# Optimization experiments

Hardware: AMD Instinct MI355X
Metric: run time of the kernel (lower is better)

## Reference

```python
import jax, jax.numpy as jnp
import numpy as np

B, T, H = 32, 512, 1024   # batch, seq, hidden
L = 512                   # max_seq_length (must be <= 512 for rel_pos_bias)
E = 2048                  # hidden * expansion_factor
S = 128                   # shared qk dim
SQRT_S = float(np.sqrt(S))
EPS = 1e-5


def setup_inputs() -> dict:
    key = jax.random.key(0)
    ks = jax.random.split(key, 9)
    return {
        "x": jax.random.normal(ks[0], (B, T, H), jnp.float32),
        "ln_w": jnp.ones((H,), jnp.float32),
        "ln_b": jnp.zeros((H,), jnp.float32),
        "uv_w": jax.random.normal(ks[1], (2 * E + S, H), jnp.float32) * 0.02,  # torch Linear [out,in]
        "uv_b": jnp.zeros((2 * E + S,), jnp.float32),
        "gamma": jax.random.uniform(ks[2], (2, S), jnp.float32),
        "beta": jax.random.uniform(ks[3], (2, S), jnp.float32),
        "w": jax.random.uniform(ks[4], (2 * L - 1,), jnp.float32),  # Toeplitz rel-pos table
        "o_w": jax.random.normal(ks[5], (H, E), jnp.float32) * 0.02,
        "o_b": jnp.zeros((H,), jnp.float32),
    }


def _rope(x):
    # x: [B, T, 2, S]; positions run along the seq dim (dim=1), faithful to GAU.rope
    half = x.shape[-1] // 2
    pos = jnp.arange(x.shape[1], dtype=x.dtype)
    # note: original uses 10000**(+i/half) (increasing freq) — keep it faithful
    inv_freq = 10000.0 ** (jnp.arange(half, dtype=x.dtype) / half)
    sinusoid = pos[:, None] * inv_freq[None, :]          # [T, half]
    sin = jnp.sin(sinusoid)[None, :, None, :]            # [1, T, 1, half]
    cos = jnp.cos(sinusoid)[None, :, None, :]
    x1, x2 = jnp.split(x, 2, axis=-1)
    return jnp.concatenate([x1 * cos - x2 * sin, x2 * cos + x1 * sin], axis=-1)


def reference(x, ln_w, ln_b, uv_w, uv_b, gamma, beta, w, o_w, o_b):
    Tq = x.shape[1]
    shortcut = x  # hidden_size == output_size -> residual
    # LayerNorm
    mu = jnp.mean(x, axis=-1, keepdims=True)
    var = jnp.mean(jnp.square(x - mu), axis=-1, keepdims=True)
    xn = (x - mu) / jnp.sqrt(var + EPS) * ln_w + ln_b
    # fused uv projection + SiLU, then split into gate u, value v, base
    uv = jax.nn.silu(xn @ uv_w.T + uv_b)                  # [B, T, 2E+S]
    u, v, base = uv[..., :E], uv[..., E:2 * E], uv[..., 2 * E:]
    base = base[:, :, None, :] * gamma[None, None] + beta  # [B, T, 2, S]
    base = _rope(base)
    q, k = base[:, :, 0, :], base[:, :, 1, :]             # [B, T, S]
    qk = jnp.einsum('bis,bjs->bij', q, k)                 # [B, T, T]
    # Toeplitz rel-pos bias: bias[i, j] = w[j - i + L - 1]
    rel = jnp.arange(Tq)[None, :] - jnp.arange(Tq)[:, None] + (L - 1)
    bias = w[rel]                                         # [T, T]
    kernel = jnp.square(jax.nn.relu(qk / SQRT_S + bias[None]))  # squared-ReLU attention
    out = u * jnp.einsum('bij,bje->bie', kernel, v)       # gated attention output [B, T, E]
    return out @ o_w.T + o_b + shortcut
```

## Files before the change

kernel.cpp:

```cpp
#include <hip/hip_runtime.h>

typedef unsigned short u16;
typedef __bf16 bf16x8 __attribute__((ext_vector_type(8)));
typedef float f32x4 __attribute__((ext_vector_type(4)));

#define B_ 32
#define T_ 512
#define H_ 1024
#define E_ 2048
#define S_ 128

__device__ inline u16 f2bf(float f) {
  union { float f; unsigned int u; } c; c.f = f;
  unsigned int u = c.u;
  unsigned int r = (u + 0x7FFFu + ((u >> 16) & 1u)) >> 16;
  return (u16)r;
}
__device__ inline float bf2f(u16 h) {
  union { unsigned int u; float f; } c; c.u = ((unsigned int)h) << 16; return c.f;
}
__device__ inline float silu_fast(float v) {
  return v * __builtin_amdgcn_rcpf(1.0f + __expf(-v));
}

__device__ inline void g2lds16(const u16* g, u16* l) {
  __builtin_amdgcn_global_load_lds(
      (const __attribute__((address_space(1))) void*)g,
      (__attribute__((address_space(3))) void*)l, 16, 0, 0);
}

__global__ __launch_bounds__(256) void ln_kernel(const float* __restrict__ x,
                                                 const float* __restrict__ lw,
                                                 const float* __restrict__ lb,
                                                 u16* __restrict__ xn) {
  int row = blockIdx.x;
  int t = threadIdx.x;
  const float4* xr = (const float4*)(x + (size_t)row * H_);
  float4 v = xr[t];
  float s = v.x + v.y + v.z + v.w;
  float ss = v.x * v.x + v.y * v.y + v.z * v.z + v.w * v.w;
  for (int off = 1; off < 64; off <<= 1) {
    s += __shfl_xor(s, off);
    ss += __shfl_xor(ss, off);
  }
  __shared__ float red[8];
  int w = t >> 6, l = t & 63;
  if (l == 0) { red[w] = s; red[4 + w] = ss; }
  __syncthreads();
  s = red[0] + red[1] + red[2] + red[3];
  ss = red[4] + red[5] + red[6] + red[7];
  float mu = s * (1.0f / H_);
  float var = ss * (1.0f / H_) - mu * mu;
  float inv = rsqrtf(var + 1e-5f);
  int i = t * 4;
  ushort4 o;
  o.x = f2bf((v.x - mu) * inv * lw[i] + lb[i]);
  o.y = f2bf((v.y - mu) * inv * lw[i + 1] + lb[i + 1]);
  o.z = f2bf((v.z - mu) * inv * lw[i + 2] + lb[i + 2]);
  o.w = f2bf((v.w - mu) * inv * lw[i + 3] + lb[i + 3]);
  *(ushort4*)(xn + (size_t)row * H_ + i) = o;
}

__global__ void cvt_kernel(const float* __restrict__ in, u16* __restrict__ out, int n4) {
  int i = blockIdx.x * 256 + threadIdx.x;
  if (i < n4) {
    float4 v = ((const float4*)in)[i];
    ushort4 o;
    o.x = f2bf(v.x); o.y = f2bf(v.y); o.z = f2bf(v.z); o.w = f2bf(v.w);
    ((ushort4*)out)[i] = o;
  }
}

__global__ __launch_bounds__(256) void rope_kernel(const float* __restrict__ base,
                                                   const float* __restrict__ gamma,
                                                   const float* __restrict__ beta,
                                                   u16* __restrict__ q,
                                                   u16* __restrict__ k) {
  int row = blockIdx.x * 4 + (threadIdx.x >> 6);
  int s = threadIdx.x & 63;
  int t = row & (T_ - 1);
  const float* bp = base + (size_t)row * S_;
  float b1 = bp[s], b2 = bp[s + 64];
  float q1 = b1 * gamma[s] + beta[s];
  float q2 = b2 * gamma[64 + s] + beta[64 + s];
  float k1 = b1 * gamma[128 + s] + beta[128 + s];
  float k2 = b2 * gamma[192 + s] + beta[192 + s];
  float invf = (float)pow(10000.0, (double)s * (1.0 / 64.0));
  float ph = (float)t * invf;
  float sn, cs;
  sincosf(ph, &sn, &cs);
  size_t o = (size_t)row * S_;
  q[o + s]      = f2bf(q1 * cs - q2 * sn);
  q[o + 64 + s] = f2bf(q2 * cs + q1 * sn);
  k[o + s]      = f2bf(k1 * cs - k2 * sn);
  k[o + 64 + s] = f2bf(k2 * cs + k1 * sn);
}

template <int MODE>
__global__ __launch_bounds__(256)
void gemm_bt(const u16* __restrict__ A, const u16* __restrict__ Bm,
             int K, long long sA, long long sB,
             void* __restrict__ o0, void* __restrict__ o1, void* __restrict__ o2,
             const void* __restrict__ c0, const void* __restrict__ c1, int nb0) {
  __shared__ __attribute__((aligned(16))) u16 lds[32768];
  u16* lsA = lds;
  u16* lsB = lds + 16384;

  const int z = blockIdx.z;
  const u16* Ab = A + (long long)z * sA;
  const u16* Bb = Bm + (long long)z * sB;
  const int m0 = blockIdx.y * 128;
  const int n0 = nb0 + blockIdx.x * 128;
  const int t = threadIdx.x;
  const int w = t >> 6, l = t & 63;
  const int quad = l >> 4, l16 = l & 15;
  const int wm = (w >> 1) * 64, wn = (w & 1) * 64;
  const int srow = t >> 4;
  const int gl = (t & 15) ^ ((t >> 4) & 7);
  const int dst_off = t * 8;
  const int rsw = l16 & 7;

  f32x4 zero = {0.f, 0.f, 0.f, 0.f};
  f32x4 acc[4][4];
  for (int mi = 0; mi < 4; ++mi)
    for (int ni = 0; ni < 4; ++ni) acc[mi][ni] = zero;

  const u16* gA = Ab + ((size_t)(m0 + srow) * K + gl * 8);
  const u16* gB = Bb + ((size_t)(n0 + srow) * K + gl * 8);
  const size_t rK16 = (size_t)16 * K;

  for (int k0 = 0; k0 < K; k0 += 128) {
    __syncthreads();
#pragma unroll
    for (int c = 0; c < 8; ++c)
      g2lds16(gA + k0 + c * rK16, &lsA[c * 2048 + dst_off]);
#pragma unroll
    for (int c = 0; c < 8; ++c)
      g2lds16(gB + k0 + c * rK16, &lsB[c * 2048 + dst_off]);
    __syncthreads();
#pragma unroll
    for (int j = 0; j < 4; ++j) {
      int pg = ((j * 4 + quad) ^ rsw) * 8;
      bf16x8 af[4], bfr[4];
      for (int i = 0; i < 4; ++i) {
        af[i]  = *(const bf16x8*)&lsA[(wm + i * 16 + l16) * 128 + pg];
        bfr[i] = *(const bf16x8*)&lsB[(wn + i * 16 + l16) * 128 + pg];
      }
      for (int mi = 0; mi < 4; ++mi)
        for (int ni = 0; ni < 4; ++ni)
          acc[mi][ni] = __builtin_amdgcn_mfma_f32_16x16x32_bf16(af[mi], bfr[ni], acc[mi][ni], 0, 0, 0);
    }
  }

  for (int mi = 0; mi < 4; ++mi) {
    for (int ni = 0; ni < 4; ++ni) {
      int n = n0 + wn + ni * 16 + l16;
      for (int r = 0; r < 4; ++r) {
        int m = m0 + wm + mi * 16 + quad * 4 + r;
        float a = acc[mi][ni][r];
        if constexpr (MODE == 1) {
          const float* wrel = (const float*)c0;
          float v = a * 0.08838834764831845f + wrel[n - m + 511];
          v = fmaxf(v, 0.0f);
          ((u16*)o0)[(size_t)z * (T_ * T_) + (size_t)m * T_ + n] = f2bf(v * v);
        }
      }
    }
  }
}

#define PH_SYNC()                                        \
  asm volatile("s_waitcnt lgkmcnt(0)" ::: "memory");     \
  __builtin_amdgcn_sched_barrier(0);                     \
  __builtin_amdgcn_s_barrier();                          \
  __builtin_amdgcn_sched_barrier(0);                     \
  __builtin_amdgcn_s_setprio(1);

#define PH_END()                                         \
  __builtin_amdgcn_s_setprio(0);

#define MM2(mA, mB)                                                                                       \
  _Pragma("unroll")                                                                                       \
  for (int ni = 0; ni < 4; ++ni) {                                                                        \
    acc[mA][ni] = __builtin_amdgcn_mfma_f32_16x16x32_bf16(af[mA][0], bfr[ni][0], acc[mA][ni], 0, 0, 0);   \
    acc[mB][ni] = __builtin_amdgcn_mfma_f32_16x16x32_bf16(af[mB][0], bfr[ni][0], acc[mB][ni], 0, 0, 0);   \
  }                                                                                                       \
  _Pragma("unroll")                                                                                       \
  for (int ni = 0; ni < 4; ++ni) {                                                                        \
    acc[mA][ni] = __builtin_amdgcn_mfma_f32_16x16x32_bf16(af[mA][1], bfr[ni][1], acc[mA][ni], 0, 0, 0);   \
    acc[mB][ni] = __builtin_amdgcn_mfma_f32_16x16x32_bf16(af[mB][1], bfr[ni][1], acc[mB][ni], 0, 0, 0);   \
  }

template <int MODE, bool XSWZ>
__global__ __launch_bounds__(512, 2)
void gemm256(const u16* __restrict__ A, const u16* __restrict__ Bm,
             int K, long long sA, long long sB,
             void* __restrict__ o0, void* __restrict__ o1, void* __restrict__ o2,
             const void* __restrict__ c0, const void* __restrict__ c1, int NB) {
  extern __shared__ u16 lds[];

  int bx = blockIdx.x, by = blockIdx.y;
  if constexpr (XSWZ) {
    int gx = gridDim.x;
    int nwg = gx * gridDim.y;
    int hh = by * gx + bx;
    int cpx = nwg >> 3;
    int lid = (hh & 7) * cpx + (hh >> 3);
    bx = lid % gx; by = lid / gx;
  }
  const int z = blockIdx.z;
  const u16* Ab = A + (long long)z * sA;
  const u16* Bb = Bm + (long long)z * sB;
  const int m0 = by * 256;
  const int n0 = bx * 256;
  const int t = threadIdx.x;
  const int w = t >> 6, ln = t & 63;
  const int quad = ln >> 4, l16 = ln & 15;
  const int wm = w >> 2, wn = w & 3;

  const int nkt = K >> 6;

  const int goff = ((t & 7) ^ ((t >> 3) & 7)) * 8;
  const u16* gA = Ab + (size_t)(m0 + (t >> 3)) * K + goff;
  const u16* gB = Bb + (size_t)(n0 + (t >> 3)) * K + goff;
  u16* ldst = lds + t * 8;
  const size_t rK64 = (size_t)64 * K;
  const size_t rK128 = (size_t)128 * K;
  const size_t hB1 = ((size_t)n0 + 256 <= (size_t)NB) ? rK128 : 0;

  auto SA = [&](int b, int h, int kt) {
    const u16* g = gA + h * rK128 + (size_t)kt * 64;
    u16* d = ldst + b * 16384 + h * 8192;
    g2lds16(g, d);
    g2lds16(g + rK64, d + 4096);
  };
  auto SB = [&](int b, int h, int kt) {
    const u16* g = gB + (h ? hB1 : 0) + (size_t)kt * 64;
    u16* d = ldst + 32768 + b * 16384 + h * 8192;
    g2lds16(g, d);
    g2lds16(g + rK64, d + 4096);
  };

  f32x4 zero = {0.f, 0.f, 0.f, 0.f};
  f32x4 acc[8][4];
#pragma unroll
  for (int mi = 0; mi < 8; ++mi)
#pragma unroll
    for (int ni = 0; ni < 4; ++ni) acc[mi][ni] = zero;

  SA(0, 0, 0); SA(0, 1, 0); SB(0, 0, 0); SB(0, 1, 0);
  if (nkt > 1) {
    SB(1, 0, 1); SB(1, 1, 1); SA(1, 0, 1);
    asm volatile("s_waitcnt vmcnt(6)" ::: "memory");
  } else {
    asm volatile("s_waitcnt vmcnt(0)" ::: "memory");
  }
  __builtin_amdgcn_s_barrier();

  const u16* lA0 = lds + wm * 8192 + l16 * 64;
  const u16* lB0 = lds + 32768 + (wn >> 1) * 8192 + ((wn & 1) * 64 + l16) * 64;
  const int pg0 = (quad ^ (l16 & 7)) * 8;
  const int pg1 = ((4 + quad) ^ (l16 & 7)) * 8;

  bf16x8 bfr[4][2];
  bf16x8 af[8][2];

  for (int kt = 0; kt < nkt; ++kt) {
    const int b = kt & 1;
    const u16* lA = lA0 + b * 16384;
    const u16* lB = lB0 + b * 16384;
    const bool s2 = (kt + 2 < nkt);

#pragma unroll
    for (int ni = 0; ni < 4; ++ni) {
      bfr[ni][0] = *(const bf16x8*)&lB[ni * 1024 + pg0];
      bfr[ni][1] = *(const bf16x8*)&lB[ni * 1024 + pg1];
    }
#pragma unroll
    for (int mi = 0; mi < 2; ++mi) {
      af[mi][0] = *(const bf16x8*)&lA[mi * 1024 + pg0];
      af[mi][1] = *(const bf16x8*)&lA[mi * 1024 + pg1];
    }
    if (kt + 1 < nkt) SA(b ^ 1, 1, kt + 1);
    PH_SYNC();
    MM2(0, 1);
    PH_END();

#pragma unroll
    for (int mi = 2; mi < 6; ++mi) {
      af[mi][0] = *(const bf16x8*)&lA[mi * 1024 + pg0];
      af[mi][1] = *(const bf16x8*)&lA[mi * 1024 + pg1];
    }
    if (s2) SB(b, 0, kt + 2);
    PH_SYNC();
    MM2(2, 3);
    PH_END();

#pragma unroll
    for (int mi = 6; mi < 8; ++mi) {
      af[mi][0] = *(const bf16x8*)&lA[mi * 1024 + pg0];
      af[mi][1] = *(const bf16x8*)&lA[mi * 1024 + pg1];
    }
    if (s2) SB(b, 1, kt + 2);
    PH_SYNC();
    MM2(4, 5);
    PH_END();

    if (s2) {
      SA(b, 0, kt + 2);
      asm volatile("s_waitcnt vmcnt(6)" ::: "memory");
    } else {
      asm volatile("s_waitcnt vmcnt(0)" ::: "memory");
    }
    __builtin_amdgcn_sched_barrier(0);
    __builtin_amdgcn_s_barrier();
    __builtin_amdgcn_sched_barrier(0);
    __builtin_amdgcn_s_setprio(1);
    MM2(6, 7);
    PH_END();
  }

  if constexpr (MODE == 0) {
    const float* uvb = (const float*)c0;
    if (n0 < E_) {
#pragma unroll
      for (int ni = 0; ni < 4; ++ni) {
        int n = n0 + wn * 64 + ni * 16 + l16;
        float bias = uvb[n];
#pragma unroll
        for (int mi = 0; mi < 8; ++mi)
#pragma unroll
          for (int r = 0; r < 4; ++r) {
            int m = m0 + wm * 128 + mi * 16 + quad * 4 + r;
            ((u16*)o0)[(size_t)m * E_ + n] = f2bf(silu_fast(acc[mi][ni][r] + bias));
          }
      }
    } else if (n0 < 2 * E_) {
      const int bb = m0 >> 9;
      const int tt0 = m0 & (T_ - 1);
      const int nv0 = n0 - E_;
#pragma unroll
      for (int ni = 0; ni < 4; ++ni) {
        int nl = wn * 64 + ni * 16 + l16;
        float bias = uvb[n0 + nl];
#pragma unroll
        for (int mi = 0; mi < 8; ++mi)
#pragma unroll
          for (int r = 0; r < 4; ++r) {
            int ml = wm * 128 + mi * 16 + quad * 4 + r;
            u16 sv = f2bf(silu_fast(acc[mi][ni][r] + bias));
            int g = ml >> 3, o = ml & 7;
            lds[nl * 256 + ((g ^ (nl & 7)) << 3) + o] = sv;
          }
      }
      __syncthreads();
      int row = t >> 1;
      u16* o1p = (u16*)o1;
      size_t gbase = ((size_t)bb * E_ + nv0 + row) * T_ + tt0;
#pragma unroll
      for (int cc = 0; cc < 16; ++cc) {
        int c = (t & 1) * 16 + cc;
        int gs = c ^ (row & 7);
        uint4 val = *(const uint4*)&lds[row * 256 + gs * 8];
        *(uint4*)&o1p[gbase + c * 8] = val;
      }
    } else {
      if (wn < 2) {
#pragma unroll
        for (int ni = 0; ni < 4; ++ni) {
          int n = n0 + wn * 64 + ni * 16 + l16;
          float bias = uvb[n];
#pragma unroll
          for (int mi = 0; mi < 8; ++mi)
#pragma unroll
            for (int r = 0; r < 4; ++r) {
              int m = m0 + wm * 128 + mi * 16 + quad * 4 + r;
              ((float*)o2)[(size_t)m * S_ + (n - 2 * E_)] = silu_fast(acc[mi][ni][r] + bias);
            }
        }
      }
    }
  } else if constexpr (MODE == 2) {
    const u16* uu = (const u16*)c0;
#pragma unroll
    for (int mi = 0; mi < 8; ++mi)
#pragma unroll
      for (int ni = 0; ni < 4; ++ni) {
        int n = n0 + wn * 64 + ni * 16 + l16;
#pragma unroll
        for (int r = 0; r < 4; ++r) {
          int m = m0 + wm * 128 + mi * 16 + quad * 4 + r;
          size_t gi = ((size_t)z * T_ + m) * E_ + n;
          float uv_ = bf2f(uu[gi]);
          ((u16*)o0)[gi] = f2bf(acc[mi][ni][r] * uv_);
        }
      }
  } else {
    const float* ob = (const float*)c0;
    const float* xs = (const float*)c1;
#pragma unroll
    for (int ni = 0; ni < 4; ++ni) {
      int n = n0 + wn * 64 + ni * 16 + l16;
      float bias = ob[n];
#pragma unroll
      for (int mi = 0; mi < 8; ++mi)
#pragma unroll
        for (int r = 0; r < 4; ++r) {
          int m = m0 + wm * 128 + mi * 16 + quad * 4 + r;
          size_t gi = (size_t)m * H_ + n;
          ((float*)o0)[gi] = acc[mi][ni][r] + bias + xs[gi];
        }
    }
  }
}

extern "C" void kernel_launch(void* const* d_in, const int* in_sizes, int n_in,
                              void* d_out, int out_size, void* d_ws, size_t ws_size,
                              hipStream_t stream) {
  const float* x     = (const float*)d_in[0];
  const float* ln_w  = (const float*)d_in[1];
  const float* ln_b  = (const float*)d_in[2];
  const float* uv_w  = (const float*)d_in[3];
  const float* uv_b  = (const float*)d_in[4];
  const float* gamma = (const float*)d_in[5];
  const float* beta  = (const float*)d_in[6];
  const float* wrel  = (const float*)d_in[7];
  const float* o_w   = (const float*)d_in[8];
  const float* o_b   = (const float*)d_in[9];

  char* ws = (char*)d_ws;
  u16*   xn   = (u16*)(ws);
  u16*   qb   = (u16*)(ws);
  u16*   kb   = (u16*)(ws + 4194304);
  u16*   km   = (u16*)(ws + 8388608);
  u16*   uvwb = (u16*)(ws + 33554432);
  u16*   owb  = (u16*)(ws + 42205184);
  u16*   u    = (u16*)(ws + 46399488);
  u16*   vt   = (u16*)(ws + 113508352);
  float* base = (float*)(ws + 180617216);
  u16*   attn = u;

  static int ldsset = -1;
  if (ldsset < 0) {
    auto* k0 = gemm256<0, true>;
    auto* k2 = gemm256<2, false>;
    auto* k3 = gemm256<3, true>;
    hipFuncSetAttribute((const void*)k0, hipFuncAttributeMaxDynamicSharedMemorySize, 131072);
    hipFuncSetAttribute((const void*)k2, hipFuncAttributeMaxDynamicSharedMemorySize, 131072);
    hipFuncSetAttribute((const void*)k3, hipFuncAttributeMaxDynamicSharedMemorySize, 131072);
    ldsset = 1;
  }

  ln_kernel<<<16384, 256, 0, stream>>>(x, ln_w, ln_b, xn);
  cvt_kernel<<<4224, 256, 0, stream>>>(uv_w, uvwb, 4224 * 1024 / 4);
  cvt_kernel<<<2048, 256, 0, stream>>>(o_w, owb, 1024 * 2048 / 4);

  gemm256<0, true><<<dim3(17, 64, 1), 512, 131072, stream>>>(
      xn, uvwb, 1024, 0, 0, u, vt, base, uv_b, nullptr, 4224);
  rope_kernel<<<4096, 256, 0, stream>>>(base, gamma, beta, qb, kb);
  gemm_bt<1><<<dim3(4, 4, 32), 256, 0, stream>>>(
      qb, kb, 128, 65536, 65536, km, nullptr, nullptr, wrel, nullptr, 0);
  gemm256<2, false><<<dim3(8, 2, 32), 512, 131072, stream>>>(
      km, vt, 512, 262144, 1048576, attn, nullptr, nullptr, u, nullptr, 1 << 30);
  gemm256<3, true><<<dim3(4, 64, 1), 512, 131072, stream>>>(
      attn, owb, 2048, 0, 0, d_out, nullptr, nullptr, o_b, x, 1 << 30);
}
```

Before: 518.4 us.

## Split base projection into separate small GEMM and stage epilogues through LDS

Moves the 128-column base projection out of the big uv GEMM, which drops its partial 17th column tile, into a separate gemm_bt launch over the remaining columns. The u-output and MODE 2 gated epilogues now stage bf16 results in swizzled LDS and write coalesced 16-byte vectors. The MODE 2 gate multiply also reads u with vector loads instead of scattered 2-byte accesses. This trades an extra kernel launch and an extra bf16 rounding of the attention accumulator (before the gate multiply) for better store coalescing.

```diff
diff --git a/kernel.cpp b/kernel.cpp
--- a/kernel.cpp
+++ b/kernel.cpp
@@ -158,7 +158,10 @@
       for (int r = 0; r < 4; ++r) {
         int m = m0 + wm + mi * 16 + quad * 4 + r;
         float a = acc[mi][ni][r];
-        if constexpr (MODE == 1) {
+        if constexpr (MODE == 0) {
+          const float* uvb = (const float*)c0;
+          ((float*)o2)[(size_t)m * S_ + (n - 2 * E_)] = silu_fast(a + uvb[n]);
+        } else if constexpr (MODE == 1) {
           const float* wrel = (const float*)c0;
           float v = a * 0.08838834764831845f + wrel[n - m + 511];
           v = fmaxf(v, 0.0f);
@@ -195,8 +198,8 @@
 __global__ __launch_bounds__(512, 2)
 void gemm256(const u16* __restrict__ A, const u16* __restrict__ Bm,
              int K, long long sA, long long sB,
-             void* __restrict__ o0, void* __restrict__ o1, void* __restrict__ o2,
-             const void* __restrict__ c0, const void* __restrict__ c1, int NB) {
+             void* __restrict__ o0, void* __restrict__ o1,
+             const void* __restrict__ c0, const void* __restrict__ c1) {
   extern __shared__ u16 lds[];
 
   int bx = blockIdx.x, by = blockIdx.y;
@@ -226,7 +229,6 @@
   u16* ldst = lds + t * 8;
   const size_t rK64 = (size_t)64 * K;
   const size_t rK128 = (size_t)128 * K;
-  const size_t hB1 = ((size_t)n0 + 256 <= (size_t)NB) ? rK128 : 0;
 
   auto SA = [&](int b, int h, int kt) {
     const u16* g = gA + h * rK128 + (size_t)kt * 64;
@@ -235,7 +237,7 @@
     g2lds16(g + rK64, d + 4096);
   };
   auto SB = [&](int b, int h, int kt) {
-    const u16* g = gB + (h ? hB1 : 0) + (size_t)kt * 64;
+    const u16* g = gB + h * rK128 + (size_t)kt * 64;
     u16* d = ldst + 32768 + b * 16384 + h * 8192;
     g2lds16(g, d);
     g2lds16(g + rK64, d + 4096);
@@ -325,17 +327,28 @@
     if (n0 < E_) {
 #pragma unroll
       for (int ni = 0; ni < 4; ++ni) {
-        int n = n0 + wn * 64 + ni * 16 + l16;
-        float bias = uvb[n];
+        int nl = wn * 64 + ni * 16 + l16;
+        float bias = uvb[n0 + nl];
+        int g = nl >> 3, o = nl & 7;
 #pragma unroll
         for (int mi = 0; mi < 8; ++mi)
 #pragma unroll
           for (int r = 0; r < 4; ++r) {
-            int m = m0 + wm * 128 + mi * 16 + quad * 4 + r;
-            ((u16*)o0)[(size_t)m * E_ + n] = f2bf(silu_fast(acc[mi][ni][r] + bias));
+            int ml = wm * 128 + mi * 16 + quad * 4 + r;
+            lds[ml * 256 + ((g ^ (ml & 7)) << 3) + o] =
+                f2bf(silu_fast(acc[mi][ni][r] + bias));
           }
       }
-    } else if (n0 < 2 * E_) {
+      __syncthreads();
+      u16* o0p = (u16*)o0;
+#pragma unroll
+      for (int cc = 0; cc < 16; ++cc) {
+        int gidx = cc * 512 + t;
+        int row = gidx >> 5, gc = gidx & 31;
+        uint4 val = *(const uint4*)&lds[row * 256 + ((gc ^ (row & 7)) << 3)];
+        *(uint4*)&o0p[(size_t)(m0 + row) * E_ + n0 + gc * 8] = val;
+      }
+    } else {
       const int bb = m0 >> 9;
       const int tt0 = m0 & (T_ - 1);
       const int nv0 = n0 - E_;
@@ -364,37 +377,36 @@
         uint4 val = *(const uint4*)&lds[row * 256 + gs * 8];
         *(uint4*)&o1p[gbase + c * 8] = val;
       }
-    } else {
-      if (wn < 2) {
-#pragma unroll
-        for (int ni = 0; ni < 4; ++ni) {
-          int n = n0 + wn * 64 + ni * 16 + l16;
-          float bias = uvb[n];
-#pragma unroll
-          for (int mi = 0; mi < 8; ++mi)
-#pragma unroll
-            for (int r = 0; r < 4; ++r) {
-              int m = m0 + wm * 128 + mi * 16 + quad * 4 + r;
-              ((float*)o2)[(size_t)m * S_ + (n - 2 * E_)] = silu_fast(acc[mi][ni][r] + bias);
-            }
+    }
+  } else if constexpr (MODE == 2) {
+#pragma unroll
+    for (int ni = 0; ni < 4; ++ni) {
+      int nl = wn * 64 + ni * 16 + l16;
+      int g = nl >> 3, o = nl & 7;
+#pragma unroll
+      for (int mi = 0; mi < 8; ++mi)
+#pragma unroll
+        for (int r = 0; r < 4; ++r) {
+          int ml = wm * 128 + mi * 16 + quad * 4 + r;
+          lds[ml * 256 + ((g ^ (ml & 7)) << 3) + o] = f2bf(acc[mi][ni][r]);
         }
-      }
-    }
-  } else if constexpr (MODE == 2) {
+    }
+    __syncthreads();
     const u16* uu = (const u16*)c0;
-#pragma unroll
-    for (int mi = 0; mi < 8; ++mi)
-#pragma unroll
-      for (int ni = 0; ni < 4; ++ni) {
-        int n = n0 + wn * 64 + ni * 16 + l16;
-#pragma unroll
-        for (int r = 0; r < 4; ++r) {
-          int m = m0 + wm * 128 + mi * 16 + quad * 4 + r;
-          size_t gi = ((size_t)z * T_ + m) * E_ + n;
-          float uv_ = bf2f(uu[gi]);
-          ((u16*)o0)[gi] = f2bf(acc[mi][ni][r] * uv_);
-        }
-      }
+    u16* o0p = (u16*)o0;
+#pragma unroll
+    for (int cc = 0; cc < 16; ++cc) {
+      int gidx = cc * 512 + t;
+      int row = gidx >> 5, gc = gidx & 31;
+      union { uint4 v; u16 h[8]; } av, uv_, rv;
+      av.v = *(const uint4*)&lds[row * 256 + ((gc ^ (row & 7)) << 3)];
+      size_t gi = ((size_t)z * T_ + m0 + row) * E_ + n0 + gc * 8;
+      uv_.v = *(const uint4*)&uu[gi];
+#pragma unroll
+      for (int k = 0; k < 8; ++k)
+        rv.h[k] = f2bf(bf2f(av.h[k]) * bf2f(uv_.h[k]));
+      *(uint4*)&o0p[gi] = rv.v;
+    }
   } else {
     const float* ob = (const float*)c0;
     const float* xs = (const float*)c1;
@@ -455,13 +467,15 @@
   cvt_kernel<<<4224, 256, 0, stream>>>(uv_w, uvwb, 4224 * 1024 / 4);
   cvt_kernel<<<2048, 256, 0, stream>>>(o_w, owb, 1024 * 2048 / 4);
 
-  gemm256<0, true><<<dim3(17, 64, 1), 512, 131072, stream>>>(
-      xn, uvwb, 1024, 0, 0, u, vt, base, uv_b, nullptr, 4224);
+  gemm256<0, true><<<dim3(16, 64, 1), 512, 131072, stream>>>(
+      xn, uvwb, 1024, 0, 0, u, vt, uv_b, nullptr);
+  gemm_bt<0><<<dim3(1, 128, 1), 256, 0, stream>>>(
+      xn, uvwb, 1024, 0, 0, nullptr, nullptr, base, uv_b, nullptr, 4096);
   rope_kernel<<<4096, 256, 0, stream>>>(base, gamma, beta, qb, kb);
   gemm_bt<1><<<dim3(4, 4, 32), 256, 0, stream>>>(
       qb, kb, 128, 65536, 65536, km, nullptr, nullptr, wrel, nullptr, 0);
   gemm256<2, false><<<dim3(8, 2, 32), 512, 131072, stream>>>(
-      km, vt, 512, 262144, 1048576, attn, nullptr, nullptr, u, nullptr, 1 << 30);
+      km, vt, 512, 262144, 1048576, attn, nullptr, u, nullptr);
   gemm256<3, true><<<dim3(4, 64, 1), 512, 131072, stream>>>(
-      attn, owb, 2048, 0, 0, d_out, nullptr, nullptr, o_b, x, 1 << 30);
-}
+      attn, owb, 2048, 0, 0, d_out, nullptr, o_b, x);
+}
```

Result: no change. 519.7 us (+0.2%).
